# Kernel optimization log

Hardware: AMD Instinct MI355X
Metric: run time of the kernel (lower is better)

## Reference

```python
import jax, jax.numpy as jnp
import numpy as np

T, B, H, K = 512, 64, 512, 16  # seq_len, batch, hidden_size, num_tags


def setup_inputs() -> dict:
    key = jax.random.key(0)
    ks = jax.random.split(key, 8)
    hidden = jax.random.normal(ks[0], (T, B, H), dtype=jnp.float32)
    W1 = jax.random.normal(ks[1], (H, H), dtype=jnp.float32) / np.float32(np.sqrt(H))
    b1 = jnp.zeros((H,), jnp.float32)
    W2 = jax.random.normal(ks[2], (H, K), dtype=jnp.float32) / np.float32(np.sqrt(H))
    b2 = jnp.zeros((K,), jnp.float32)
    transition = jax.random.normal(ks[3], (K, K), dtype=jnp.float32)
    lens = jax.random.randint(ks[4], (B,), T // 2, T + 1)  # valid lengths in [T/2, T]
    tags = jax.random.randint(ks[5], (T, B), 0, K)
    return dict(hidden=hidden, W1=W1, b1=b1, W2=W2, b2=b2,
                transition=transition, lens=lens, tags=tags)


def reference(hidden, W1, b1, W2, b2, transition, lens, tags):
    # Emission MLP (dropout is identity in eval): Linear -> ReLU -> Linear
    h = jax.nn.relu(hidden @ W1 + b1)          # [T, B, H]
    em = h @ W2 + b2                           # [T, B, K]

    # ---- forward (partition) score: linear-chain logsumexp DP ----
    def step(alpha, e_t):
        # alpha: [B, K] over prev tags; transition[curr, prev]
        a = jax.nn.logsumexp(alpha[:, None, :] + transition[None, :, :], axis=-1) + e_t
        return a, a

    alpha0 = em[0]
    _, alphas = jax.lax.scan(step, alpha0, em[1:])
    alphas = jnp.concatenate([alpha0[None], alphas], axis=0)            # [T, B, K]
    last = jnp.take_along_axis(alphas, (lens - 1)[None, :, None], axis=0)[0]  # [B, K]
    fwd_score = jax.nn.logsumexp(last, axis=-1)                          # [B]

    # ---- gold path score ----
    em_path = jnp.take_along_axis(em, tags[:, :, None], axis=-1)[..., 0]  # [T, B]
    trans_path = transition[tags[1:], tags[:-1]]                          # [T-1, B]
    steps = em_path.at[1:].add(trans_path)
    cum = jnp.cumsum(steps, axis=0)                                       # [T, B]
    gold = jnp.take_along_axis(cum, (lens - 1)[None, :], axis=0)[0]       # [B]

    return (fwd_score - gold).sum()
```

## Files before the change

### kernel.cpp

```cpp
#include <hip/hip_runtime.h>
#include <hip/hip_bf16.h>

#define TT 512
#define BB 64
#define HH 512
#define KK 16

typedef __attribute__((ext_vector_type(8))) short bf16x8;
typedef __attribute__((ext_vector_type(4))) short bf16x4;
typedef __attribute__((ext_vector_type(4))) float f32x4;

#define MFMA_K16(A, B, C) __builtin_amdgcn_mfma_f32_16x16x16bf16_1k(A, B, C, 0, 0, 0)

__device__ __forceinline__ unsigned short f2bf(float f) {
    union { __hip_bfloat16 h; unsigned short u; } cvt;
    cvt.h = __float2bfloat16(f);
    return cvt.u;
}

__device__ __forceinline__ short rne_bf(float x) {
    unsigned u = __float_as_uint(x);
    u += 0x7fffu + ((u >> 16) & 1u);
    return (short)(u >> 16);
}

__device__ __forceinline__ float bf2f(short s) {
    return __uint_as_float(((unsigned)(unsigned short)s) << 16);
}

__global__ void prep_kernel(const float* __restrict__ W1, const float* __restrict__ W2,
                            unsigned short* __restrict__ W1t, unsigned short* __restrict__ W2t,
                            float* __restrict__ out) {
    const int bi = blockIdx.x, tx = threadIdx.x;
    if (bi < 64) {
        __shared__ float Ls[64][65];
        const int ti = bi & 7, tj = bi >> 3;
        const int r0 = ti * 64, c0 = tj * 64;
        const int r = tx >> 4, c4 = (tx & 15) * 4;
#pragma unroll
        for (int i = 0; i < 4; ++i) {
            float4 v = *(const float4*)(W1 + (size_t)(r0 + r + 16 * i) * HH + c0 + c4);
            Ls[c4 + 0][r + 16 * i] = v.x;
            Ls[c4 + 1][r + 16 * i] = v.y;
            Ls[c4 + 2][r + 16 * i] = v.z;
            Ls[c4 + 3][r + 16 * i] = v.w;
        }
        __syncthreads();
        const int rn = tx >> 4, k4 = (tx & 15) * 4;
#pragma unroll
        for (int i = 0; i < 4; ++i) {
            const int n = rn + 16 * i;
            ushort4 o;
            o.x = f2bf(Ls[n][k4 + 0]);
            o.y = f2bf(Ls[n][k4 + 1]);
            o.z = f2bf(Ls[n][k4 + 2]);
            o.w = f2bf(Ls[n][k4 + 3]);
            *(ushort4*)(W1t + (size_t)(c0 + n) * HH + r0 + k4) = o;
        }
    } else {
        if (tx == 0) out[0] = 0.0f;
        for (int idx = tx; idx < 16 * HH; idx += 256) {
            const int n = idx >> 9, k = idx & 511;
            W2t[idx] = f2bf(W2[k * KK + n]);
        }
    }
}

__global__ __launch_bounds__(256, 2)
void em_kernel(const float* __restrict__ hidden, const unsigned short* __restrict__ W1t,
               const float* __restrict__ b1, const unsigned short* __restrict__ W2t,
               const float* __restrict__ b2, float* __restrict__ em) {
    __shared__ unsigned short W2ts[16 * 520];
    __shared__ __align__(16) unsigned char stage[37888];
    unsigned short* As = (unsigned short*)stage;
    unsigned short* Bs = (unsigned short*)(stage + 5120);
    unsigned short* Hb = (unsigned short*)stage;

    const int tx = threadIdx.x;
    const int w = tx >> 6, lane = tx & 63;
    const int q = lane >> 4, nl = lane & 15;
    const int wm = w >> 1, wn = w & 1;
    const int row0 = blockIdx.x * 64;

    for (int i = tx; i < 16 * 64; i += 256) {
        const int n = i >> 6, kc = i & 63;
        *(bf16x8*)(W2ts + n * 520 + kc * 8) = *(const bf16x8*)(W2t + n * HH + kc * 8);
    }

    f32x4 acc[2][16];
#pragma unroll
    for (int mt = 0; mt < 2; ++mt)
#pragma unroll
        for (int nt = 0; nt < 16; ++nt) acc[mt][nt] = (f32x4){0.f, 0.f, 0.f, 0.f};

    for (int kt = 0; kt < 16; ++kt) {
        const int k0 = kt * 32;
        __syncthreads();
        {
            const int r = tx >> 2, c8 = (tx & 3) * 8;
            const float* src = hidden + (size_t)(row0 + r) * HH + k0 + c8;
            float4 v0 = *(const float4*)(src);
            float4 v1 = *(const float4*)(src + 4);
            bf16x8 o;
            o[0] = (short)f2bf(v0.x); o[1] = (short)f2bf(v0.y);
            o[2] = (short)f2bf(v0.z); o[3] = (short)f2bf(v0.w);
            o[4] = (short)f2bf(v1.x); o[5] = (short)f2bf(v1.y);
            o[6] = (short)f2bf(v1.z); o[7] = (short)f2bf(v1.w);
            *(bf16x8*)(As + r * 40 + c8) = o;
        }
#pragma unroll
        for (int it = 0; it < 8; ++it) {
            const int c = it * 256 + tx;
            const int n = c >> 2, slot = c & 3;
            const int kc = slot ^ ((n >> 1) & 3);
            __builtin_amdgcn_global_load_lds(
                (const __attribute__((address_space(1))) void*)(W1t + (size_t)n * HH + k0 + kc * 8),
                (__attribute__((address_space(3))) void*)(Bs + c * 8),
                16, 0, 0);
        }
        __syncthreads();
        bf16x8 af[2];
#pragma unroll
        for (int mt = 0; mt < 2; ++mt)
            af[mt] = *(const bf16x8*)(As + (32 * wm + 16 * mt + nl) * 40 + q * 8);
#pragma unroll
        for (int nt = 0; nt < 16; ++nt) {
            const int n = 256 * wn + 16 * nt + nl;
            const int slot = q ^ ((n >> 1) & 3);
            bf16x8 bf = *(const bf16x8*)(Bs + n * 32 + slot * 8);
            acc[0][nt] = __builtin_amdgcn_mfma_f32_16x16x32_bf16(af[0], bf, acc[0][nt], 0, 0, 0);
            acc[1][nt] = __builtin_amdgcn_mfma_f32_16x16x32_bf16(af[1], bf, acc[1][nt], 0, 0, 0);
        }
    }

    f32x4 acc2 = (f32x4){0.f, 0.f, 0.f, 0.f};
    for (int c = 0; c < 2; ++c) {
        __syncthreads();
        if (wn == c) {
#pragma unroll
            for (int nt = 0; nt < 16; ++nt) {
                const float bv = b1[c * 256 + 16 * nt + nl];
#pragma unroll
                for (int mt = 0; mt < 2; ++mt) {
#pragma unroll
                    for (int r = 0; r < 4; ++r) {
                        float v = acc[mt][nt][r] + bv;
                        v = v > 0.f ? v : 0.f;
                        const int row = 32 * wm + 16 * mt + q * 4 + r;
                        Hb[row * 264 + nt * 16 + nl] = f2bf(v);
                    }
                }
            }
        }
        __syncthreads();
#pragma unroll
        for (int ks = 0; ks < 8; ++ks) {
            bf16x8 a2 = *(const bf16x8*)(Hb + (16 * w + nl) * 264 + ks * 32 + q * 8);
            bf16x8 b2f = *(const bf16x8*)(W2ts + nl * 520 + c * 256 + ks * 32 + q * 8);
            acc2 = __builtin_amdgcn_mfma_f32_16x16x32_bf16(a2, b2f, acc2, 0, 0, 0);
        }
    }
#pragma unroll
    for (int r = 0; r < 4; ++r) {
        const int row = row0 + 16 * w + q * 4 + r;
        em[(size_t)row * KK + nl] = acc2[r] + b2[nl];
    }
}

__global__ void gold_kernel(const float* __restrict__ em, const float* __restrict__ trans,
                            const int* __restrict__ lens, const int* __restrict__ tags,
                            float* __restrict__ out) {
    __shared__ float trs[256];
    __shared__ float red[4];
    const int tid = threadIdx.x;
    trs[tid] = __logf(bf2f(rne_bf(__expf(trans[tid]))));
    __syncthreads();
    const int idx = blockIdx.x * 256 + tid;
    const int t = idx >> 6, b = idx & 63;
    const int L = lens[b];
    float v = 0.0f;
    if (t < L) {
        const int tg = tags[t * BB + b];
        v = em[((size_t)t * BB + b) * KK + tg];
        if (t > 0) v += trs[tg * 16 + tags[(t - 1) * BB + b]];
    }
#pragma unroll
    for (int dd = 1; dd < 64; dd <<= 1) v += __shfl_xor(v, dd, 64);
    if ((tid & 63) == 0) red[tid >> 6] = v;
    __syncthreads();
    if (tid == 0) atomicAdd(out, -(red[0] + red[1] + red[2] + red[3]));
}

__global__ void chunk_kernel(const float* __restrict__ em, const float* __restrict__ trans,
                             const int* __restrict__ lens,
                             float* __restrict__ Pfull, float* __restrict__ Cfull,
                             float* __restrict__ Ppart, float* __restrict__ Cpart) {
    const int tx = threadIdx.x;
    const int id = blockIdx.x * 4 + (tx >> 6);
    const int lane = tx & 63, q = lane >> 4, col = lane & 15;
    const int b = id >> 3, c = id & 7;

    float mf[4];
    {
        float4 tv = *(const float4*)(trans + col * 16 + 4 * q);
        mf[0] = bf2f(rne_bf(__expf(tv.x)));
        mf[1] = bf2f(rne_bf(__expf(tv.y)));
        mf[2] = bf2f(rne_bf(__expf(tv.z)));
        mf[3] = bf2f(rne_bf(__expf(tv.w)));
    }
    const int Lm1 = lens[b] - 1;
    const int tb0 = 64 * c;

    float ebuf[8];
#pragma unroll
    for (int i = 0; i < 8; ++i)
        ebuf[i] = em[(size_t)((tb0 + i) * BB + b) * KK + col];

    bf16x4 gb;
#pragma unroll
    for (int i = 0; i < 4; ++i)
        gb[i] = (4 * q + i == col) ? rne_bf(1.0f) : (short)0;

    const f32x4 zc = (f32x4){0.f, 0.f, 0.f, 0.f};
    f32x4 d = (f32x4){0.f, 0.f, 0.f, 0.f};
    float K = 1.0f, rk = 1.0f, lk = 0.0f, Cacc = 0.0f;

    for (int sb = 0; sb < 64; sb += 8) {
        const bool refill = (sb < 56);
#pragma unroll
        for (int s8 = 0; s8 < 8; ++s8) {
            const int t = tb0 + sb + s8;
            const float eraw = ebuf[s8];
            if (refill)
                ebuf[s8] = em[(size_t)((t + 8) * BB + b) * KK + col];
            float ev = __expf(eraw);
            if ((s8 & 3) == 0 && (sb + s8) >= 4) {
                ev *= rk;
                Cacc += lk;
            }
            bf16x4 af;
            af[0] = rne_bf(ev * mf[0]); af[1] = rne_bf(ev * mf[1]);
            af[2] = rne_bf(ev * mf[2]); af[3] = rne_bf(ev * mf[3]);
            if (s8 == 0) {
                if (sb == 0 && c == 0) {
#pragma unroll
                    for (int i = 0; i < 4; ++i)
                        af[i] = (4 * q + i == col) ? rne_bf(ev) : (short)0;
                }
            }
            d = MFMA_K16(af, gb, zc);
            if ((s8 & 3) == 1) {
                K = __shfl(d[0], 0, 64);
                const float Km = fmaxf(K, 1e-30f);
                rk = 1.0f / Km;
                lk = __logf(Km);
            }
            if (t == Lm1) {
#pragma unroll
                for (int r = 0; r < 4; ++r)
                    Ppart[b * 256 + (4 * q + r) * 16 + col] = d[r];
                if (lane == 0) Cpart[b] = Cacc;
            }
            gb[0] = rne_bf(d[0]); gb[1] = rne_bf(d[1]);
            gb[2] = rne_bf(d[2]); gb[3] = rne_bf(d[3]);
        }
    }
#pragma unroll
    for (int r = 0; r < 4; ++r)
        Pfull[(size_t)(b * 8 + c) * 256 + (4 * q + r) * 16 + col] = d[r];
    if (lane == 0) Cfull[b * 8 + c] = Cacc;
}

__global__ void combine_kernel(const int* __restrict__ lens,
                               const float* __restrict__ Pfull, const float* __restrict__ Cfull,
                               const float* __restrict__ Ppart, const float* __restrict__ Cpart,
                               float* __restrict__ out) {
    const int lane = threadIdx.x;
    const int grp = lane >> 4, j = lane & 15;
    const int b = blockIdx.x * 4 + grp;
    const int base = grp << 4;
    const int cstar = (lens[b] - 1) >> 6;

    float g = 1.0f, acc = 0.0f;
    for (int c = 0; c < 8; ++c) {
        const bool act = (c <= cstar);
        const float* P = (c < cstar) ? (Pfull + (size_t)(b * 8 + c) * 256)
                                     : (Ppart + b * 256);
        float gn = 0.0f;
#pragma unroll
        for (int k = 0; k < 16; ++k) {
            const float gk = __shfl(g, base + k, 64);
            gn += P[j * 16 + k] * gk;
        }
        if (act) {
            float m = gn;
#pragma unroll
            for (int dd = 1; dd < 16; dd <<= 1) m = fmaxf(m, __shfl_xor(m, dd, 64));
            g = gn / m;
            acc += __logf(m) + ((c < cstar) ? Cfull[b * 8 + c] : Cpart[b]);
        }
    }
    float ssum = g;
#pragma unroll
    for (int dd = 1; dd < 16; dd <<= 1) ssum += __shfl_xor(ssum, dd, 64);
    const float fwd = acc + __logf(ssum);
    if (j == 0) atomicAdd(out, fwd);
}

extern "C" void kernel_launch(void* const* d_in, const int* in_sizes, int n_in,
                              void* d_out, int out_size, void* d_ws, size_t ws_size,
                              hipStream_t stream) {
    const float* hidden = (const float*)d_in[0];
    const float* W1     = (const float*)d_in[1];
    const float* b1     = (const float*)d_in[2];
    const float* W2     = (const float*)d_in[3];
    const float* b2     = (const float*)d_in[4];
    const float* trans  = (const float*)d_in[5];
    const int*   lens   = (const int*)d_in[6];
    const int*   tags   = (const int*)d_in[7];
    float* out = (float*)d_out;

    char* ws = (char*)d_ws;
    float* em = (float*)ws;
    unsigned short* W1t = (unsigned short*)(ws + 2097152);
    unsigned short* W2t = (unsigned short*)(ws + 2621440);
    float* Pfull = (float*)(ws + 2637824);
    float* Cfull = (float*)(ws + 3162112);
    float* Ppart = (float*)(ws + 3164160);
    float* Cpart = (float*)(ws + 3229696);

    prep_kernel<<<65, 256, 0, stream>>>(W1, W2, W1t, W2t, out);
    em_kernel<<<512, 256, 0, stream>>>(hidden, W1t, b1, W2t, b2, em);
    gold_kernel<<<128, 256, 0, stream>>>(em, trans, lens, tags, out);
    chunk_kernel<<<128, 256, 0, stream>>>(em, trans, lens, Pfull, Cfull, Ppart, Cpart);
    combine_kernel<<<16, 64, 0, stream>>>(lens, Pfull, Cfull, Ppart, Cpart, out);
}
```

Measured before the change: 165.2 us.

## Split forward scan into 32 chunks and fuse gold kernel into scan launch

The forward-score scan now uses 32 chunks of 16 timesteps per batch row instead of 8 chunks of 64. This shortens the serial per-wave dependency chain and launches 512 scan blocks instead of 128, giving more parallelism on the GPU. The gold-path kernel is merged into the same launch as extra blocks, which removes one kernel launch. In exchange, the combine kernel has a longer serial chain of 32 matrix-vector steps, and the workspace offsets are moved to fit the larger chunk arrays.

Measured after the change: 160.0 us. -3.2%, faster.

```diff
diff --git a/kernel.cpp b/kernel.cpp
--- a/kernel.cpp
+++ b/kernel.cpp
@@ -5,6 +5,9 @@
 #define BB 64
 #define HH 512
 #define KK 16
+
+#define NCH 32
+#define CST (TT / NCH)
 
 typedef __attribute__((ext_vector_type(8))) short bf16x8;
 typedef __attribute__((ext_vector_type(4))) short bf16x4;
@@ -167,38 +170,38 @@
     }
 }
 
-__global__ void gold_kernel(const float* __restrict__ em, const float* __restrict__ trans,
-                            const int* __restrict__ lens, const int* __restrict__ tags,
-                            float* __restrict__ out) {
+__global__ void scan_gold_kernel(const float* __restrict__ em, const float* __restrict__ trans,
+                                 const int* __restrict__ lens, const int* __restrict__ tags,
+                                 float* __restrict__ Pfull, float* __restrict__ Cfull,
+                                 float* __restrict__ Ppart, float* __restrict__ Cpart,
+                                 float* __restrict__ out) {
     __shared__ float trs[256];
     __shared__ float red[4];
-    const int tid = threadIdx.x;
-    trs[tid] = __logf(bf2f(rne_bf(__expf(trans[tid]))));
-    __syncthreads();
-    const int idx = blockIdx.x * 256 + tid;
-    const int t = idx >> 6, b = idx & 63;
-    const int L = lens[b];
-    float v = 0.0f;
-    if (t < L) {
-        const int tg = tags[t * BB + b];
-        v = em[((size_t)t * BB + b) * KK + tg];
-        if (t > 0) v += trs[tg * 16 + tags[(t - 1) * BB + b]];
-    }
-#pragma unroll
-    for (int dd = 1; dd < 64; dd <<= 1) v += __shfl_xor(v, dd, 64);
-    if ((tid & 63) == 0) red[tid >> 6] = v;
-    __syncthreads();
-    if (tid == 0) atomicAdd(out, -(red[0] + red[1] + red[2] + red[3]));
-}
-
-__global__ void chunk_kernel(const float* __restrict__ em, const float* __restrict__ trans,
-                             const int* __restrict__ lens,
-                             float* __restrict__ Pfull, float* __restrict__ Cfull,
-                             float* __restrict__ Ppart, float* __restrict__ Cpart) {
     const int tx = threadIdx.x;
+
+    if (blockIdx.x >= 512) {
+        trs[tx] = __logf(bf2f(rne_bf(__expf(trans[tx]))));
+        __syncthreads();
+        const int idx = (blockIdx.x - 512) * 256 + tx;
+        const int t = idx >> 6, b = idx & 63;
+        const int L = lens[b];
+        float v = 0.0f;
+        if (t < L) {
+            const int tg = tags[t * BB + b];
+            v = em[((size_t)t * BB + b) * KK + tg];
+            if (t > 0) v += trs[tg * 16 + tags[(t - 1) * BB + b]];
+        }
+#pragma unroll
+        for (int dd = 1; dd < 64; dd <<= 1) v += __shfl_xor(v, dd, 64);
+        if ((tx & 63) == 0) red[tx >> 6] = v;
+        __syncthreads();
+        if (tx == 0) atomicAdd(out, -(red[0] + red[1] + red[2] + red[3]));
+        return;
+    }
+
     const int id = blockIdx.x * 4 + (tx >> 6);
     const int lane = tx & 63, q = lane >> 4, col = lane & 15;
-    const int b = id >> 3, c = id & 7;
+    const int b = id >> 5, c = id & 31;
 
     float mf[4];
     {
@@ -209,7 +212,7 @@
         mf[3] = bf2f(rne_bf(__expf(tv.w)));
     }
     const int Lm1 = lens[b] - 1;
-    const int tb0 = 64 * c;
+    const int tb0 = CST * c;
 
     float ebuf[8];
 #pragma unroll
@@ -225,8 +228,8 @@
     f32x4 d = (f32x4){0.f, 0.f, 0.f, 0.f};
     float K = 1.0f, rk = 1.0f, lk = 0.0f, Cacc = 0.0f;
 
-    for (int sb = 0; sb < 64; sb += 8) {
-        const bool refill = (sb < 56);
+    for (int sb = 0; sb < CST; sb += 8) {
+        const bool refill = (sb < CST - 8);
 #pragma unroll
         for (int s8 = 0; s8 < 8; ++s8) {
             const int t = tb0 + sb + s8;
@@ -267,8 +270,8 @@
     }
 #pragma unroll
     for (int r = 0; r < 4; ++r)
-        Pfull[(size_t)(b * 8 + c) * 256 + (4 * q + r) * 16 + col] = d[r];
-    if (lane == 0) Cfull[b * 8 + c] = Cacc;
+        Pfull[(size_t)(b * NCH + c) * 256 + (4 * q + r) * 16 + col] = d[r];
+    if (lane == 0) Cfull[b * NCH + c] = Cacc;
 }
 
 __global__ void combine_kernel(const int* __restrict__ lens,
@@ -279,12 +282,12 @@
     const int grp = lane >> 4, j = lane & 15;
     const int b = blockIdx.x * 4 + grp;
     const int base = grp << 4;
-    const int cstar = (lens[b] - 1) >> 6;
+    const int cstar = (lens[b] - 1) / CST;
 
     float g = 1.0f, acc = 0.0f;
-    for (int c = 0; c < 8; ++c) {
+    for (int c = 0; c < NCH; ++c) {
         const bool act = (c <= cstar);
-        const float* P = (c < cstar) ? (Pfull + (size_t)(b * 8 + c) * 256)
+        const float* P = (c < cstar) ? (Pfull + (size_t)(b * NCH + c) * 256)
                                      : (Ppart + b * 256);
         float gn = 0.0f;
 #pragma unroll
@@ -297,7 +300,7 @@
 #pragma unroll
             for (int dd = 1; dd < 16; dd <<= 1) m = fmaxf(m, __shfl_xor(m, dd, 64));
             g = gn / m;
-            acc += __logf(m) + ((c < cstar) ? Cfull[b * 8 + c] : Cpart[b]);
+            acc += __logf(m) + ((c < cstar) ? Cfull[b * NCH + c] : Cpart[b]);
         }
     }
     float ssum = g;
@@ -325,13 +328,13 @@
     unsigned short* W1t = (unsigned short*)(ws + 2097152);
     unsigned short* W2t = (unsigned short*)(ws + 2621440);
     float* Pfull = (float*)(ws + 2637824);
-    float* Cfull = (float*)(ws + 3162112);
-    float* Ppart = (float*)(ws + 3164160);
-    float* Cpart = (float*)(ws + 3229696);
+    float* Cfull = (float*)(ws + 4734976);
+    float* Ppart = (float*)(ws + 4743168);
+    float* Cpart = (float*)(ws + 4808704);
 
     prep_kernel<<<65, 256, 0, stream>>>(W1, W2, W1t, W2t, out);
     em_kernel<<<512, 256, 0, stream>>>(hidden, W1t, b1, W2t, b2, em);
-    gold_kernel<<<128, 256, 0, stream>>>(em, trans, lens, tags, out);
-    chunk_kernel<<<128, 256, 0, stream>>>(em, trans, lens, Pfull, Cfull, Ppart, Cpart);
+    scan_gold_kernel<<<640, 256, 0, stream>>>(em, trans, lens, tags,
+                                              Pfull, Cfull, Ppart, Cpart, out);
     combine_kernel<<<16, 64, 0, stream>>>(lens, Pfull, Cfull, Ppart, Cpart, out);
 }
```
